# Optimization experiments

Hardware: AMD Instinct MI355X
Metric: run time of the kernel (lower is better)

The kernel has to match this reference:

```python
import jax, jax.numpy as jnp
import numpy as np

V, E, D, B, L1, L2, C, NL = 32000, 300, 256, 64, 128, 128, 3, 10
BN_EPS = 1e-3  # tf.layers.batch_normalization default epsilon
BN_SCALE = 1.0 / np.sqrt(1.0 + BN_EPS)  # inference BN with moving mean=0, var=1


def setup_inputs() -> dict:
    key = jax.random.key(0)
    ks = iter(jax.random.split(key, 32))
    g = lambda shape, s=0.05: jax.random.normal(next(ks), shape, jnp.float32) * s
    inp = dict(
        embed_table=g((V, E), 1.0),
        W1_first=g((E, D)),            # layer 1 linear-BN-ReLU-1 (input dim = embed dim)
        W1_rest=g((NL - 1, D, D)),     # layers 2..10 linear-BN-ReLU-1
        b1=jnp.zeros((NL, D)),
        bn1_g=jnp.ones((NL, D)), bn1_b=jnp.zeros((NL, D)),
        W2=g((NL, 2 * D, D)),          # linear-BN-ReLU-2 on [x, aligned] concat
        b2=jnp.zeros((NL, D)),
        bn2_g=jnp.ones((NL, D)), bn2_b=jnp.zeros((NL, D)),
        Wg=g((NL, D, D)), bg=jnp.zeros((NL, D)),  # sigmoid gate
        Wf1=g((4 * D, 4 * D), 0.01), bf1=jnp.zeros((4 * D,)),
        Wf2=g((4 * D, 4 * D), 0.01), bf2=jnp.zeros((4 * D,)),
        Wout=g((4 * D, C)), bout=jnp.zeros((C,)),
        x1_ids=jax.random.randint(next(ks), (B, L1), 0, V, dtype=jnp.int32),
        x2_ids=jax.random.randint(next(ks), (B, L2), 0, V, dtype=jnp.int32),
    )
    return inp


def _lbr(x, W, b, g, be):
    # linear -> BN (inference: moving mean 0, var 1) -> ReLU
    y = jnp.dot(x, W) + b
    y = g * (y * BN_SCALE) + be
    return jax.nn.relu(y)


def _block(x1, x2):
    # pairwise squared euclidean distance: |a-b|^2 = |a|^2 + |b|^2 - 2 a.b
    sq1 = jnp.sum(x1 * x1, -1)                                  # [B,L1]
    sq2 = jnp.sum(x2 * x2, -1)                                  # [B,L2]
    edist = sq1[:, :, None] + sq2[:, None, :] \
        - 2.0 * jnp.einsum('bid,bjd->bij', x1, x2)              # [B,L1,L2]
    att = 1.0 / (1.0 + edist)
    # alpha = softmax(att^T) @ x1 ; beta = softmax(att) @ x2
    alpha = jnp.einsum('bji,bid->bjd',
                       jax.nn.softmax(jnp.swapaxes(att, 1, 2), axis=-1), x1)  # [B,L2,D]
    beta = jnp.einsum('bij,bjd->bid', jax.nn.softmax(att, axis=-1), x2)       # [B,L1,D]
    return alpha, beta


def reference(embed_table, W1_first, W1_rest, b1, bn1_g, bn1_b,
              W2, b2, bn2_g, bn2_b, Wg, bg,
              Wf1, bf1, Wf2, bf2, Wout, bout, x1_ids, x2_ids):
    x1 = embed_table[x1_ids]  # [B,L1,E]
    x2 = embed_table[x2_ids]  # [B,L2,E]
    for i in range(NL):
        W1 = W1_first if i == 0 else W1_rest[i - 1]
        h1 = _lbr(x1, W1, b1[i], bn1_g[i], bn1_b[i])
        h2 = _lbr(x2, W1, b1[i], bn1_g[i], bn1_b[i])
        alpha, beta = _block(h1, h2)
        v1 = _lbr(jnp.concatenate([h1, beta], -1), W2[i], b2[i], bn2_g[i], bn2_b[i])
        v2 = _lbr(jnp.concatenate([h2, alpha], -1), W2[i], b2[i], bn2_g[i], bn2_b[i])
        g1 = jax.nn.sigmoid(jnp.dot(h1, Wg[i]) + bg[i])
        g2 = jax.nn.sigmoid(jnp.dot(h2, Wg[i]) + bg[i])
        x1 = v1 * g1 + h1 * (1.0 - g1)
        x2 = v2 * g2 + h2 * (1.0 - g2)
    v = jnp.concatenate([x1.max(1), x2.max(1), x1.sum(1), x2.sum(1)], -1)  # [B,4D]
    t = jax.nn.relu(jnp.dot(v, Wf1) + bf1)   # op.linear default activation (ReLU); dropout off
    t = jax.nn.relu(jnp.dot(t, Wf2) + bf2)
    return jnp.dot(t, Wout) + bout           # logits [B,C]
```

## Files before the change

kernel.cpp:

```cpp
#include <hip/hip_runtime.h>
#include <hip/hip_bf16.h>
#include <cstddef>

#define NB 64
#define LL 128
#define EE 300
#define DD 256
#define NLAYERS 10
#define MROWS (NB * LL)

static constexpr float BN_SC = 0.9995003746877562f;

typedef unsigned short u16;
typedef __attribute__((ext_vector_type(4))) unsigned short us4;
typedef __attribute__((ext_vector_type(8))) unsigned short us8;
typedef __attribute__((ext_vector_type(8))) short bfrag;
typedef __attribute__((ext_vector_type(4))) float f4;

#define MFMA_B16(a, b, c) __builtin_amdgcn_mfma_f32_16x16x32_bf16(a, b, c, 0, 0, 0)

__device__ __forceinline__ u16 f2bf(float x) {
  union { float f; unsigned u; } v; v.f = x;
  unsigned r = v.u + 0x7FFFu + ((v.u >> 16) & 1u);
  return (u16)(r >> 16);
}
__device__ __forceinline__ float bf2f(u16 s) {
  union { unsigned u; float f; } v; v.u = (unsigned)s << 16;
  return v.f;
}
__device__ __forceinline__ float4 ld4(const float* p) { return *(const float4*)p; }

__device__ __forceinline__ void async16(void* lds, const void* g) {
  __builtin_amdgcn_global_load_lds(
      (const __attribute__((address_space(1))) unsigned int*)g,
      (__attribute__((address_space(3))) unsigned int*)lds, 16, 0, 0);
}

__device__ __forceinline__ int swz64(int row, int colbyte) {
  return (row * 128 + colbyte) ^ ((row & 7) << 4);
}
__device__ __forceinline__ bfrag ldsT(const u16* T, int row, int colbyte) {
  return *(const bfrag*)((const char*)T + swz64(row, colbyte));
}

__device__ __forceinline__ void stage128x64(const u16* __restrict__ src, int ld,
                                            int r0, int k0, u16* lds, int t) {
  const int w = t >> 6;
#pragma unroll
  for (int j = 0; j < 4; ++j) {
    const int c = j * 256 + t;
    const int row = c >> 3, part = c & 7;
    const int sp = part ^ (row & 7);
    async16((char*)lds + j * 4096 + w * 1024,
            src + (size_t)(r0 + row) * ld + k0 + sp * 8);
  }
}
__device__ __forceinline__ void stage64x64(const u16* __restrict__ src, int ld,
                                           int r0, int k0, u16* lds, int t) {
  const int w = t >> 6;
#pragma unroll
  for (int j = 0; j < 2; ++j) {
    const int c = j * 256 + t;
    const int row = c >> 3, part = c & 7;
    const int sp = part ^ (row & 7);
    async16((char*)lds + j * 4096 + w * 1024,
            src + (size_t)(r0 + row) * ld + k0 + sp * 8);
  }
}

__device__ __forceinline__ void step_k64(const u16* As, const u16* Bs, int wm,
                                         int wn, int fr, int fq, f4 acc[4][2]) {
#pragma unroll
  for (int ks2 = 0; ks2 < 2; ++ks2) {
    bfrag a[4], b[2];
#pragma unroll
    for (int i = 0; i < 4; ++i)
      a[i] = ldsT(As, wm * 64 + i * 16 + fr, ks2 * 64 + fq * 16);
#pragma unroll
    for (int j = 0; j < 2; ++j)
      b[j] = ldsT(Bs, wn * 32 + j * 16 + fr, ks2 * 64 + fq * 16);
#pragma unroll
    for (int i = 0; i < 4; ++i)
#pragma unroll
      for (int j = 0; j < 2; ++j) acc[i][j] = MFMA_B16(a[i], b[j], acc[i][j]);
  }
}

__device__ __forceinline__ void step2_k64(const u16* As, const u16* B2s,
                                          const u16* Bgs, int wm, int wn,
                                          int fr, int fq, f4 accv[4][2],
                                          f4 accg[4][2]) {
#pragma unroll
  for (int ks2 = 0; ks2 < 2; ++ks2) {
    bfrag a[4], b2[2], bg[2];
#pragma unroll
    for (int i = 0; i < 4; ++i)
      a[i] = ldsT(As, wm * 64 + i * 16 + fr, ks2 * 64 + fq * 16);
#pragma unroll
    for (int j = 0; j < 2; ++j) {
      b2[j] = ldsT(B2s, wn * 32 + j * 16 + fr, ks2 * 64 + fq * 16);
      bg[j] = ldsT(Bgs, wn * 32 + j * 16 + fr, ks2 * 64 + fq * 16);
    }
#pragma unroll
    for (int i = 0; i < 4; ++i)
#pragma unroll
      for (int j = 0; j < 2; ++j) {
        accv[i][j] = MFMA_B16(a[i], b2[j], accv[i][j]);
        accg[i][j] = MFMA_B16(a[i], bg[j], accg[i][j]);
      }
  }
}

__device__ __forceinline__ bfrag gfrag(const u16* __restrict__ p, int ld, int row, int k) {
  return *(const bfrag*)(p + (size_t)row * ld + k);
}

__device__ __forceinline__ int eswz(int row, int colbyte) {
  return (row * 256 + colbyte) ^ ((row & 7) << 4);
}
__device__ __forceinline__ bfrag ldsE(const u16* E, int row, int colbyte) {
  return *(const bfrag*)((const char*)E + eswz(row, colbyte));
}

__device__ void txw_tile(const float* __restrict__ src, u16* __restrict__ dst,
                         int K, int N, int Kpad, int k0, int n0, int t,
                         float (*tileS)[65]) {
  __syncthreads();
  {
    const int kr = t >> 2, nc = (t & 3) * 16;
    const int k = k0 + kr;
#pragma unroll
    for (int j = 0; j < 16; j += 4) {
      float4 v = (k < K) ? ld4(src + (size_t)k * N + n0 + nc + j)
                         : make_float4(0.f, 0.f, 0.f, 0.f);
      tileS[kr][nc + j + 0] = v.x; tileS[kr][nc + j + 1] = v.y;
      tileS[kr][nc + j + 2] = v.z; tileS[kr][nc + j + 3] = v.w;
    }
  }
  __syncthreads();
  {
    const int nr = t >> 2, kc = (t & 3) * 16;
    us8 o0, o1;
#pragma unroll
    for (int j = 0; j < 8; ++j) {
      o0[j] = f2bf(tileS[kc + j][nr]);
      o1[j] = f2bf(tileS[kc + 8 + j][nr]);
    }
    u16* d = dst + (size_t)(n0 + nr) * Kpad + k0 + kc;
    *(us8*)d = o0;
    *(us8*)(d + 8) = o1;
  }
}

__global__ __launch_bounds__(256)
void k_prep(const float* __restrict__ W1f, const float* __restrict__ W1r,
            const float* __restrict__ W2, const float* __restrict__ Wg,
            const float* __restrict__ Wf1, const float* __restrict__ Wf2,
            u16* __restrict__ Wt1f, u16* __restrict__ Wt1r,
            u16* __restrict__ Wt2, u16* __restrict__ Wtg,
            u16* __restrict__ Wf1t, u16* __restrict__ Wf2t,
            const float* __restrict__ embed, const int* __restrict__ ids1,
            const int* __restrict__ ids2, u16* __restrict__ X1,
            u16* __restrict__ X2, u16* __restrict__ VPh, u16* __restrict__ VPl) {
  __shared__ float tileS[64][65];
  const int t = threadIdx.x;
  const int blk = blockIdx.x, nblk = gridDim.x;
  for (int it = blk; it < 20; it += nblk)
    txw_tile(W1f, Wt1f, 300, 256, 320, (it % 5) * 64, (it / 5) * 64, t, tileS);
  for (int it = blk; it < 144; it += nblk) {
    const int l = it / 16, r = it % 16;
    txw_tile(W1r + (size_t)l * 65536, Wt1r + (size_t)l * 65536, 256, 256, 256,
             (r % 4) * 64, (r / 4) * 64, t, tileS);
  }
  for (int it = blk; it < 320; it += nblk) {
    const int l = it / 32, r = it % 32;
    txw_tile(W2 + (size_t)l * 131072, Wt2 + (size_t)l * 131072, 512, 256, 512,
             (r % 8) * 64, (r / 8) * 64, t, tileS);
  }
  for (int it = blk; it < 160; it += nblk) {
    const int l = it / 16, r = it % 16;
    txw_tile(Wg + (size_t)l * 65536, Wtg + (size_t)l * 65536, 256, 256, 256,
             (r % 4) * 64, (r / 4) * 64, t, tileS);
  }
  for (int it = blk; it < 256; it += nblk)
    txw_tile(Wf1, Wf1t, 1024, 1024, 1024, (it % 16) * 64, (it / 16) * 64, t, tileS);
  for (int it = blk; it < 256; it += nblk)
    txw_tile(Wf2, Wf2t, 1024, 1024, 1024, (it % 16) * 64, (it / 16) * 64, t, tileS);
  for (int g = blk; g < 4096; g += nblk) {
    const int side = g & 1;
    const int* ids = side ? ids2 : ids1;
    u16* E = side ? X2 : X1;
    const int row = (g >> 1) * 4 + (t >> 6);
    const int lane = t & 63;
    const float* src = embed + (size_t)ids[row] * EE;
    u16* dst = E + (size_t)row * 320;
#pragma unroll
    for (int j = 0; j < 5; ++j) {
      const int c = lane + 64 * j;
      dst[c] = f2bf(c < EE ? src[c] : 0.f);
    }
  }
  for (int it = blk; it < 128; it += nblk) {
    const int arr = it & 1, row = 64 + (it >> 1);
    u16* dst = (arr ? VPl : VPh) + (size_t)row * 1024;
#pragma unroll
    for (int j = 0; j < 4; ++j) dst[t * 4 + j] = 0;
  }
}

__global__ __launch_bounds__(256, 2)
void mfma_lbr(const u16* __restrict__ A0, const u16* __restrict__ A1, int lda,
              int K, const u16* __restrict__ Wt, const float* __restrict__ bias,
              const float* __restrict__ gam, const float* __restrict__ bet,
              u16* __restrict__ O0, u16* __restrict__ O1,
              u16* __restrict__ HTa, u16* __restrict__ HTb,
              float* __restrict__ SQPa, float* __restrict__ SQPb) {
  const int side = blockIdx.z;
  const u16* A = side ? A1 : A0;
  u16* O = side ? O1 : O0;
  u16* HT = side ? HTb : HTa;
  float* SQP = side ? SQPb : SQPa;
  __shared__ u16 As[2][128 * 64], Bs[2][64 * 64];
  const int t = threadIdx.x;
  const int m0 = blockIdx.x * 128, n0 = blockIdx.y * 64;
  const int lane = t & 63, w = t >> 6, wm = w >> 1, wn = w & 1;
  const int fr = lane & 15, fq = lane >> 4;
  f4 acc[4][2] = {};
  const int nt = K / 64;
  stage128x64(A, lda, m0, 0, As[0], t);
  stage64x64(Wt, K, n0, 0, Bs[0], t);
  __syncthreads();
  for (int ks = 0; ks < nt; ++ks) {
    const int cur = ks & 1;
    if (ks + 1 < nt) {
      stage128x64(A, lda, m0, (ks + 1) * 64, As[cur ^ 1], t);
      stage64x64(Wt, K, n0, (ks + 1) * 64, Bs[cur ^ 1], t);
    }
    step_k64(As[cur], Bs[cur], wm, wn, fr, fq, acc);
    __syncthreads();
  }
  const int b = m0 >> 7;
  float rsq[4][4] = {};
#pragma unroll
  for (int nj = 0; nj < 2; ++nj) {
    const int n = n0 + wn * 32 + nj * 16 + fr;
    const float sc = gam[n] * BN_SC, bi = bias[n], be = bet[n];
#pragma unroll
    for (int mi = 0; mi < 4; ++mi) {
      const int m = m0 + wm * 64 + mi * 16 + fq * 4;
      us4 pk;
#pragma unroll
      for (int r = 0; r < 4; ++r) {
        const float x = sc * (acc[mi][nj][r] + bi) + be;
        const u16 hb = f2bf(fmaxf(x, 0.f));
        O[(size_t)(m + r) * DD + n] = hb;
        pk[r] = hb;
        const float h = bf2f(hb);
        rsq[mi][r] += h * h;
      }
      *(us4*)&HT[((size_t)b * DD + n) * LL + (m & 127)] = pk;
    }
  }
#pragma unroll
  for (int mi = 0; mi < 4; ++mi)
#pragma unroll
    for (int r = 0; r < 4; ++r) {
      float v = rsq[mi][r];
      v += __shfl_xor(v, 1, 64); v += __shfl_xor(v, 2, 64);
      v += __shfl_xor(v, 4, 64); v += __shfl_xor(v, 8, 64);
      rsq[mi][r] = v;
    }
  if (fr == 0) {
    const int p = blockIdx.y * 2 + wn;
#pragma unroll
    for (int mi = 0; mi < 4; ++mi)
#pragma unroll
      for (int r = 0; r < 4; ++r)
        SQP[(size_t)p * MROWS + m0 + wm * 64 + mi * 16 + fq * 4 + r] = rsq[mi][r];
  }
}

__global__ __launch_bounds__(256, 2)
void attf(const u16* __restrict__ H1, const u16* __restrict__ H2,
          const float* __restrict__ SQP1, const float* __restrict__ SQP2,
          const u16* __restrict__ HT1, const u16* __restrict__ HT2,
          u16* __restrict__ BETA, u16* __restrict__ ALPHA) {
  const int b = blockIdx.x, nh = blockIdx.y, side = blockIdx.z;
  __shared__ u16 Elds[128 * 128];
  __shared__ float sqs[2][128], rowp[2][128], colp[2][128];
  const int t = threadIdx.x, lane = t & 63, w = t >> 6;
  const int wm = w >> 1, wn = w & 1;
  const int fr = lane & 15, fq = lane >> 4;
  const int r0 = b * LL;
  if (t < 128) {
    float s = 0.f;
#pragma unroll
    for (int p = 0; p < 8; ++p) s += SQP1[(size_t)p * MROWS + r0 + t];
    sqs[0][t] = s;
  } else {
    const int u = t - 128;
    float s = 0.f;
#pragma unroll
    for (int p = 0; p < 8; ++p) s += SQP2[(size_t)p * MROWS + r0 + u];
    sqs[1][u] = s;
  }
  f4 acc[4][4] = {};
#pragma unroll
  for (int ks = 0; ks < 8; ++ks) {
    bfrag a[4], bv[4];
#pragma unroll
    for (int mi = 0; mi < 4; ++mi)
      a[mi] = gfrag(H1, DD, r0 + wm * 64 + mi * 16 + fr, ks * 32 + fq * 8);
#pragma unroll
    for (int nj = 0; nj < 4; ++nj)
      bv[nj] = gfrag(H2, DD, r0 + wn * 64 + nj * 16 + fr, ks * 32 + fq * 8);
#pragma unroll
    for (int mi = 0; mi < 4; ++mi)
#pragma unroll
      for (int nj = 0; nj < 4; ++nj) acc[mi][nj] = MFMA_B16(a[mi], bv[nj], acc[mi][nj]);
  }
  __syncthreads();
  float rp[4][4] = {}, cp[4] = {};
#pragma unroll
  for (int nj = 0; nj < 4; ++nj) {
    const int n = wn * 64 + nj * 16 + fr;
    const float s2 = sqs[1][n];
#pragma unroll
    for (int mi = 0; mi < 4; ++mi) {
      const int m = wm * 64 + mi * 16 + fq * 4;
#pragma unroll
      for (int r = 0; r < 4; ++r) {
        const float d = sqs[0][m + r] + s2 - 2.f * acc[mi][nj][r];
        const float e = __expf(1.f / (1.f + d));
        acc[mi][nj][r] = e;
        rp[mi][r] += e;
        cp[nj] += e;
      }
    }
  }
#pragma unroll
  for (int mi = 0; mi < 4; ++mi)
#pragma unroll
    for (int r = 0; r < 4; ++r) {
      float v = rp[mi][r];
      v += __shfl_xor(v, 1, 64); v += __shfl_xor(v, 2, 64);
      v += __shfl_xor(v, 4, 64); v += __shfl_xor(v, 8, 64);
      rp[mi][r] = v;
    }
#pragma unroll
  for (int nj = 0; nj < 4; ++nj) {
    float v = cp[nj];
    v += __shfl_xor(v, 16, 64); v += __shfl_xor(v, 32, 64);
    cp[nj] = v;
  }
  if (fr == 0)
#pragma unroll
    for (int mi = 0; mi < 4; ++mi)
#pragma unroll
      for (int r = 0; r < 4; ++r)
        rowp[wn][wm * 64 + mi * 16 + fq * 4 + r] = rp[mi][r];
  if (fq == 0)
#pragma unroll
    for (int nj = 0; nj < 4; ++nj)
      colp[wm][wn * 64 + nj * 16 + fr] = cp[nj];
  __syncthreads();
  if (side == 0) {
#pragma unroll
    for (int nj = 0; nj < 4; ++nj) {
      const int n = wn * 64 + nj * 16 + fr;
#pragma unroll
      for (int mi = 0; mi < 4; ++mi) {
        const int m = wm * 64 + mi * 16 + fq * 4;
#pragma unroll
        for (int r = 0; r < 4; ++r) {
          const float riv = 1.f / (rowp[0][m + r] + rowp[1][m + r]);
          *(u16*)((char*)Elds + eswz(m + r, n * 2)) = f2bf(acc[mi][nj][r] * riv);
        }
      }
    }
  } else {
#pragma unroll
    for (int nj = 0; nj < 4; ++nj) {
      const int n = wn * 64 + nj * 16 + fr;
      const float civ = 1.f / (colp[0][n] + colp[1][n]);
#pragma unroll
      for (int mi = 0; mi < 4; ++mi) {
        const int m = wm * 64 + mi * 16 + fq * 4;
        us4 pk;
#pragma unroll
        for (int r = 0; r < 4; ++r) pk[r] = f2bf(acc[mi][nj][r] * civ);
        *(us4*)((char*)Elds + eswz(n, m * 2)) = pk;
      }
    }
  }
  __syncthreads();
  const u16* HT = side ? HT1 : HT2;
  f4 pv[4][4] = {};
#pragma unroll
  for (int ks = 0; ks < 4; ++ks) {
    bfrag a[4], bv[4];
#pragma unroll
    for (int mi = 0; mi < 4; ++mi)
      a[mi] = ldsE(Elds, wm * 64 + mi * 16 + fr, ks * 64 + fq * 16);
#pragma unroll
    for (int nj = 0; nj < 4; ++nj)
      bv[nj] = gfrag(HT, LL, b * DD + nh * 128 + wn * 64 + nj * 16 + fr, ks * 32 + fq * 8);
#pragma unroll
    for (int mi = 0; mi < 4; ++mi)
#pragma unroll
      for (int nj = 0; nj < 4; ++nj) pv[mi][nj] = MFMA_B16(a[mi], bv[nj], pv[mi][nj]);
  }
  u16* O = side ? ALPHA : BETA;
#pragma unroll
  for (int nj = 0; nj < 4; ++nj) {
    const int n = nh * 128 + wn * 64 + nj * 16 + fr;
#pragma unroll
    for (int mi = 0; mi < 4; ++mi) {
      const int m = wm * 64 + mi * 16 + fq * 4;
#pragma unroll
      for (int r = 0; r < 4; ++r)
        O[(size_t)(r0 + m + r) * DD + n] = f2bf(pv[mi][nj][r]);
    }
  }
}

__global__ __launch_bounds__(256, 2)
void mfma_vg(const u16* __restrict__ Hbf1, const u16* __restrict__ Hbf2,
             const u16* __restrict__ BETA, const u16* __restrict__ ALPHA,
             const u16* __restrict__ Wt2, const u16* __restrict__ Wtg,
             const float* __restrict__ b2, const float* __restrict__ g2,
             const float* __restrict__ be2, const float* __restrict__ bgv,
             u16* __restrict__ X0, u16* __restrict__ X1p, int dopool,
             u16* __restrict__ VPh, u16* __restrict__ VPl) {
  const int side = blockIdx.z;
  const u16* H = side ? Hbf2 : Hbf1;
  const u16* CC = side ? ALPHA : BETA;
  u16* X = side ? X1p : X0;
  const int m0 = blockIdx.x * 128, n0 = blockIdx.y * 64;
  __shared__ u16 As[2][128 * 64], B2s[2][64 * 64], Bgs[2][64 * 64];
  __shared__ float pmx[2][64], psm[2][64];
  const int t = threadIdx.x;
  const int lane = t & 63, w = t >> 6, wm = w >> 1, wn = w & 1;
  const int fr = lane & 15, fq = lane >> 4;
  f4 accv[4][2] = {}, accg[4][2] = {};
  stage128x64(H, DD, m0, 0, As[0], t);
  stage64x64(Wt2, 2 * DD, n0, 0, B2s[0], t);
  stage64x64(Wtg, DD, n0, 0, Bgs[0], t);
  __syncthreads();
  for (int ks = 0; ks < 8; ++ks) {
    const int cur = ks & 1;
    if (ks + 1 < 8) {
      const u16* Asrc = (ks + 1 < 4) ? H : CC;
      stage128x64(Asrc, DD, m0, ((ks + 1) & 3) * 64, As[cur ^ 1], t);
      stage64x64(Wt2, 2 * DD, n0, (ks + 1) * 64, B2s[cur ^ 1], t);
      if (ks + 1 < 4) stage64x64(Wtg, DD, n0, (ks + 1) * 64, Bgs[cur ^ 1], t);
    }
    if (ks < 4)
      step2_k64(As[cur], B2s[cur], Bgs[cur], wm, wn, fr, fq, accv, accg);
    else
      step_k64(As[cur], B2s[cur], wm, wn, fr, fq, accv);
    __syncthreads();
  }
  float pmax[2] = {-1e30f, -1e30f}, psum[2] = {0.f, 0.f};
#pragma unroll
  for (int nj = 0; nj < 2; ++nj) {
    const int n = n0 + wn * 32 + nj * 16 + fr;
    const float sc = g2[n] * BN_SC, bi = b2[n], be = be2[n], bgn = bgv[n];
#pragma unroll
    for (int mi = 0; mi < 4; ++mi) {
      const int m = m0 + wm * 64 + mi * 16 + fq * 4;
#pragma unroll
      for (int r = 0; r < 4; ++r) {
        const float v = fmaxf(sc * (accv[mi][nj][r] + bi) + be, 0.f);
        const float g = 1.f / (1.f + __expf(-(accg[mi][nj][r] + bgn)));
        const float h = bf2f(H[(size_t)(m + r) * DD + n]);
        const u16 xb = f2bf(v * g + h * (1.f - g));
        X[(size_t)(m + r) * DD + n] = xb;
        if (dopool) {
          const float xv = bf2f(xb);
          pmax[nj] = fmaxf(pmax[nj], xv);
          psum[nj] += xv;
        }
      }
    }
  }
  if (dopool) {
#pragma unroll
    for (int nj = 0; nj < 2; ++nj) {
      float mx = pmax[nj], sm = psum[nj];
      mx = fmaxf(mx, __shfl_xor(mx, 16, 64)); sm += __shfl_xor(sm, 16, 64);
      mx = fmaxf(mx, __shfl_xor(mx, 32, 64)); sm += __shfl_xor(sm, 32, 64);
      if (fq == 0) {
        pmx[wm][wn * 32 + nj * 16 + fr] = mx;
        psm[wm][wn * 32 + nj * 16 + fr] = sm;
      }
    }
    __syncthreads();
    if (t < 64) {
      const float mx = fmaxf(pmx[0][t], pmx[1][t]);
      const float sm = psm[0][t] + psm[1][t];
      const int b = m0 >> 7;
      const int col = n0 + t;
      const u16 mh = f2bf(mx);
      VPh[(size_t)b * 1024 + side * 256 + col] = mh;
      VPl[(size_t)b * 1024 + side * 256 + col] = f2bf(mx - bf2f(mh));
      const u16 sh = f2bf(sm);
      VPh[(size_t)b * 1024 + (2 + side) * 256 + col] = sh;
      VPl[(size_t)b * 1024 + (2 + side) * 256 + col] = f2bf(sm - bf2f(sh));
    }
  }
}

__global__ __launch_bounds__(256, 2)
void mlp_sk(const u16* __restrict__ Ah, const u16* __restrict__ Al,
            const u16* __restrict__ Wt, float* __restrict__ PART) {
  const int n0 = blockIdx.x * 128;
  const int k0 = blockIdx.y * 128;
  const int t = threadIdx.x, lane = t & 63, w = t >> 6;
  const int wm = w >> 1, wn = w & 1;
  const int fr = lane & 15, fq = lane >> 4;
  f4 acc[4][4] = {};
#pragma unroll
  for (int ks = 0; ks < 4; ++ks) {
    bfrag ah[4], al[4], bv[4];
#pragma unroll
    for (int mi = 0; mi < 4; ++mi) {
      ah[mi] = gfrag(Ah, 1024, wm * 64 + mi * 16 + fr, k0 + ks * 32 + fq * 8);
      al[mi] = gfrag(Al, 1024, wm * 64 + mi * 16 + fr, k0 + ks * 32 + fq * 8);
    }
#pragma unroll
    for (int nj = 0; nj < 4; ++nj)
      bv[nj] = gfrag(Wt, 1024, n0 + wn * 64 + nj * 16 + fr, k0 + ks * 32 + fq * 8);
#pragma unroll
    for (int mi = 0; mi < 4; ++mi)
#pragma unroll
      for (int nj = 0; nj < 4; ++nj) {
        acc[mi][nj] = MFMA_B16(ah[mi], bv[nj], acc[mi][nj]);
        acc[mi][nj] = MFMA_B16(al[mi], bv[nj], acc[mi][nj]);
      }
  }
#pragma unroll
  for (int nj = 0; nj < 4; ++nj) {
    const int n = n0 + wn * 64 + nj * 16 + fr;
#pragma unroll
    for (int mi = 0; mi < 4; ++mi) {
      const int m = wm * 64 + mi * 16 + fq * 4;
#pragma unroll
      for (int r = 0; r < 4; ++r)
        PART[((size_t)blockIdx.y * 128 + m + r) * 1024 + n] = acc[mi][nj][r];
    }
  }
}

__global__ __launch_bounds__(512)
void mlp_comb(const float* __restrict__ P, const float* __restrict__ bias,
              u16* __restrict__ Oh, u16* __restrict__ Ol) {
#pragma unroll
  for (int e = 0; e < 8; ++e) {
    const int idx = blockIdx.x * 4096 + e * 512 + threadIdx.x;
    const int col = idx & 1023;
    float s = bias[col];
#pragma unroll
    for (int p = 0; p < 8; ++p) s += P[(size_t)p * 131072 + idx];
    s = fmaxf(s, 0.f);
    const u16 h = f2bf(s);
    Oh[idx] = h;
    Ol[idx] = f2bf(s - bf2f(h));
  }
}

__global__ __launch_bounds__(512)
void mlp_comb_out(const float* __restrict__ P, const float* __restrict__ bias,
                  const float* __restrict__ Wout, const float* __restrict__ bout,
                  float* __restrict__ out) {
  __shared__ float red[4][8][3];
  const int t = threadIdx.x;
  float a[4][3] = {};
#pragma unroll
  for (int e = 0; e < 8; ++e) {
    const int idx = blockIdx.x * 4096 + e * 512 + t;
    const int col = idx & 1023;
    float s = bias[col];
#pragma unroll
    for (int p = 0; p < 8; ++p) s += P[(size_t)p * 131072 + idx];
    s = fmaxf(s, 0.f);
    const int lr = e >> 1;
    a[lr][0] = fmaf(s, Wout[col * 3 + 0], a[lr][0]);
    a[lr][1] = fmaf(s, Wout[col * 3 + 1], a[lr][1]);
    a[lr][2] = fmaf(s, Wout[col * 3 + 2], a[lr][2]);
  }
  const int lane = t & 63, w = t >> 6;
#pragma unroll
  for (int lr = 0; lr < 4; ++lr)
#pragma unroll
    for (int c = 0; c < 3; ++c) {
      float v = a[lr][c];
#pragma unroll
      for (int off = 32; off > 0; off >>= 1) v += __shfl_down(v, off, 64);
      if (lane == 0) red[lr][w][c] = v;
    }
  __syncthreads();
  if (t < 12) {
    const int lr = t / 3, c = t % 3;
    float s = bout[c];
#pragma unroll
    for (int w8 = 0; w8 < 8; ++w8) s += red[lr][w8][c];
    out[(blockIdx.x * 4 + lr) * 3 + c] = s;
  }
}

extern "C" void kernel_launch(void* const* d_in, const int* in_sizes, int n_in,
                              void* d_out, int out_size, void* d_ws, size_t ws_size,
                              hipStream_t stream) {
  (void)in_sizes; (void)n_in; (void)out_size; (void)ws_size;
  const float* embed = (const float*)d_in[0];
  const float* W1f   = (const float*)d_in[1];
  const float* W1r   = (const float*)d_in[2];
  const float* b1    = (const float*)d_in[3];
  const float* bn1g  = (const float*)d_in[4];
  const float* bn1b  = (const float*)d_in[5];
  const float* W2    = (const float*)d_in[6];
  const float* b2    = (const float*)d_in[7];
  const float* bn2g  = (const float*)d_in[8];
  const float* bn2b  = (const float*)d_in[9];
  const float* Wg    = (const float*)d_in[10];
  const float* bg    = (const float*)d_in[11];
  const float* Wf1   = (const float*)d_in[12];
  const float* bf1   = (const float*)d_in[13];
  const float* Wf2   = (const float*)d_in[14];
  const float* bf2   = (const float*)d_in[15];
  const float* Wout  = (const float*)d_in[16];
  const float* bout  = (const float*)d_in[17];
  const int* ids1    = (const int*)d_in[18];
  const int* ids2    = (const int*)d_in[19];

  char* wsp = (char*)d_ws;
  auto alloc = [&](size_t bytes) {
    char* p = wsp;
    wsp += (bytes + 255) & ~(size_t)255;
    return p;
  };
  u16* Hbf1  = (u16*)alloc((size_t)MROWS * DD * 2);
  u16* Hbf2  = (u16*)alloc((size_t)MROWS * DD * 2);
  u16* HT1   = (u16*)alloc((size_t)MROWS * DD * 2);
  u16* HT2   = (u16*)alloc((size_t)MROWS * DD * 2);
  u16* Xbf1  = (u16*)alloc((size_t)MROWS * 320 * 2);
  u16* Xbf2  = (u16*)alloc((size_t)MROWS * 320 * 2);
  u16* BETAb = (u16*)alloc((size_t)MROWS * DD * 2);
  u16* ALPHAb= (u16*)alloc((size_t)MROWS * DD * 2);
  float* SQP1= (float*)alloc((size_t)8 * MROWS * 4);
  float* SQP2= (float*)alloc((size_t)8 * MROWS * 4);
  u16* Wt1f  = (u16*)alloc((size_t)DD * 320 * 2);
  u16* Wt1r  = (u16*)alloc((size_t)9 * DD * DD * 2);
  u16* Wt2   = (u16*)alloc((size_t)10 * DD * 2 * DD * 2);
  u16* Wtg   = (u16*)alloc((size_t)10 * DD * DD * 2);
  u16* Wf1t  = (u16*)alloc((size_t)1024 * 1024 * 2);
  u16* Wf2t  = (u16*)alloc((size_t)1024 * 1024 * 2);
  u16* VPh   = (u16*)alloc((size_t)128 * 1024 * 2);
  u16* VPl   = (u16*)alloc((size_t)128 * 1024 * 2);
  u16* T1h   = (u16*)alloc((size_t)128 * 1024 * 2);
  u16* T1l   = (u16*)alloc((size_t)128 * 1024 * 2);
  float* PART1 = (float*)alloc((size_t)8 * 128 * 1024 * 4);
  float* PART2 = (float*)alloc((size_t)8 * 128 * 1024 * 4);

  k_prep<<<512, 256, 0, stream>>>(W1f, W1r, W2, Wg, Wf1, Wf2,
                                  Wt1f, Wt1r, Wt2, Wtg, Wf1t, Wf2t,
                                  embed, ids1, ids2, Xbf1, Xbf2, VPh, VPl);

  for (int i = 0; i < NLAYERS; ++i) {
    const u16* Wt1 = (i == 0) ? Wt1f : (Wt1r + (size_t)(i - 1) * DD * DD);
    const int K1 = (i == 0) ? 320 : DD;
    mfma_lbr<<<dim3(MROWS / 128, 4, 2), 256, 0, stream>>>(
        Xbf1, Xbf2, K1, K1, Wt1, b1 + i * DD, bn1g + i * DD, bn1b + i * DD,
        Hbf1, Hbf2, HT1, HT2, SQP1, SQP2);
    attf<<<dim3(NB, 2, 2), 256, 0, stream>>>(Hbf1, Hbf2, SQP1, SQP2, HT1, HT2,
                                             BETAb, ALPHAb);
    mfma_vg<<<dim3(MROWS / 128, 4, 2), 256, 0, stream>>>(
        Hbf1, Hbf2, BETAb, ALPHAb, Wt2 + (size_t)i * DD * 2 * DD,
        Wtg + (size_t)i * DD * DD, b2 + i * DD, bn2g + i * DD, bn2b + i * DD,
        bg + i * DD, Xbf1, Xbf2, (i == NLAYERS - 1) ? 1 : 0, VPh, VPl);
  }
  mlp_sk<<<dim3(8, 8), 256, 0, stream>>>(VPh, VPl, Wf1t, PART1);
  mlp_comb<<<32, 512, 0, stream>>>(PART1, bf1, T1h, T1l);
  mlp_sk<<<dim3(8, 8), 256, 0, stream>>>(T1h, T1l, Wf2t, PART2);
  mlp_comb_out<<<16, 512, 0, stream>>>(PART2, bf2, Wout, bout, (float*)d_out);
}
```

Baseline: 491.1 us.

## Triple-buffer mfma_lbr staging and drop split-K from the final MLP

In mfma_lbr, staging moves from double to triple buffering. Two K tiles are prefetched ahead, with explicit vmcnt waits and a single barrier per step, so global loads overlap more with MFMA work. The final MLP also drops split-K: each of 8 blocks now runs the full K=1024 reduction and applies bias and ReLU in-kernel, and a small per-row kernel computes the output projection. This removes the partial-sum buffers and the combine kernels, but leaves only 8 blocks doing long serial K loops, so the MLP may lose parallelism.

```diff
diff --git a/kernel.cpp b/kernel.cpp
--- a/kernel.cpp
+++ b/kernel.cpp
@@ -220,7 +220,7 @@
   u16* O = side ? O1 : O0;
   u16* HT = side ? HTb : HTa;
   float* SQP = side ? SQPb : SQPa;
-  __shared__ u16 As[2][128 * 64], Bs[2][64 * 64];
+  __shared__ u16 As[3][128 * 64], Bs[3][64 * 64];
   const int t = threadIdx.x;
   const int m0 = blockIdx.x * 128, n0 = blockIdx.y * 64;
   const int lane = t & 63, w = t >> 6, wm = w >> 1, wn = w & 1;
@@ -229,15 +229,18 @@
   const int nt = K / 64;
   stage128x64(A, lda, m0, 0, As[0], t);
   stage64x64(Wt, K, n0, 0, Bs[0], t);
-  __syncthreads();
+  stage128x64(A, lda, m0, 64, As[1], t);
+  stage64x64(Wt, K, n0, 64, Bs[1], t);
   for (int ks = 0; ks < nt; ++ks) {
-    const int cur = ks & 1;
-    if (ks + 1 < nt) {
-      stage128x64(A, lda, m0, (ks + 1) * 64, As[cur ^ 1], t);
-      stage64x64(Wt, K, n0, (ks + 1) * 64, Bs[cur ^ 1], t);
-    }
-    step_k64(As[cur], Bs[cur], wm, wn, fr, fq, acc);
-    __syncthreads();
+    if (ks < nt - 1) asm volatile("s_waitcnt vmcnt(6)" ::: "memory");
+    else             asm volatile("s_waitcnt vmcnt(0)" ::: "memory");
+    __builtin_amdgcn_sched_barrier(0);
+    __builtin_amdgcn_s_barrier();
+    if (ks + 2 < nt) {
+      stage128x64(A, lda, m0, (ks + 2) * 64, As[(ks + 2) % 3], t);
+      stage64x64(Wt, K, n0, (ks + 2) * 64, Bs[(ks + 2) % 3], t);
+    }
+    step_k64(As[ks % 3], Bs[ks % 3], wm, wn, fr, fq, acc);
   }
   const int b = m0 >> 7;
   float rsq[4][4] = {};
@@ -512,25 +515,26 @@
 }
 
 __global__ __launch_bounds__(256, 2)
-void mlp_sk(const u16* __restrict__ Ah, const u16* __restrict__ Al,
-            const u16* __restrict__ Wt, float* __restrict__ PART) {
+void mlp_full(const u16* __restrict__ Ah, const u16* __restrict__ Al,
+              const u16* __restrict__ Wt, const float* __restrict__ bias,
+              u16* __restrict__ Oh, u16* __restrict__ Ol,
+              float* __restrict__ Of) {
   const int n0 = blockIdx.x * 128;
-  const int k0 = blockIdx.y * 128;
   const int t = threadIdx.x, lane = t & 63, w = t >> 6;
   const int wm = w >> 1, wn = w & 1;
   const int fr = lane & 15, fq = lane >> 4;
   f4 acc[4][4] = {};
-#pragma unroll
-  for (int ks = 0; ks < 4; ++ks) {
+#pragma unroll 4
+  for (int ks = 0; ks < 32; ++ks) {
     bfrag ah[4], al[4], bv[4];
 #pragma unroll
     for (int mi = 0; mi < 4; ++mi) {
-      ah[mi] = gfrag(Ah, 1024, wm * 64 + mi * 16 + fr, k0 + ks * 32 + fq * 8);
-      al[mi] = gfrag(Al, 1024, wm * 64 + mi * 16 + fr, k0 + ks * 32 + fq * 8);
+      ah[mi] = gfrag(Ah, 1024, wm * 64 + mi * 16 + fr, ks * 32 + fq * 8);
+      al[mi] = gfrag(Al, 1024, wm * 64 + mi * 16 + fr, ks * 32 + fq * 8);
     }
 #pragma unroll
     for (int nj = 0; nj < 4; ++nj)
-      bv[nj] = gfrag(Wt, 1024, n0 + wn * 64 + nj * 16 + fr, k0 + ks * 32 + fq * 8);
+      bv[nj] = gfrag(Wt, 1024, n0 + wn * 64 + nj * 16 + fr, ks * 32 + fq * 8);
 #pragma unroll
     for (int mi = 0; mi < 4; ++mi)
 #pragma unroll
@@ -542,71 +546,49 @@
 #pragma unroll
   for (int nj = 0; nj < 4; ++nj) {
     const int n = n0 + wn * 64 + nj * 16 + fr;
+    const float bi = bias[n];
 #pragma unroll
     for (int mi = 0; mi < 4; ++mi) {
       const int m = wm * 64 + mi * 16 + fq * 4;
 #pragma unroll
-      for (int r = 0; r < 4; ++r)
-        PART[((size_t)blockIdx.y * 128 + m + r) * 1024 + n] = acc[mi][nj][r];
-    }
-  }
-}
-
-__global__ __launch_bounds__(512)
-void mlp_comb(const float* __restrict__ P, const float* __restrict__ bias,
-              u16* __restrict__ Oh, u16* __restrict__ Ol) {
-#pragma unroll
-  for (int e = 0; e < 8; ++e) {
-    const int idx = blockIdx.x * 4096 + e * 512 + threadIdx.x;
-    const int col = idx & 1023;
-    float s = bias[col];
-#pragma unroll
-    for (int p = 0; p < 8; ++p) s += P[(size_t)p * 131072 + idx];
-    s = fmaxf(s, 0.f);
-    const u16 h = f2bf(s);
-    Oh[idx] = h;
-    Ol[idx] = f2bf(s - bf2f(h));
-  }
-}
-
-__global__ __launch_bounds__(512)
-void mlp_comb_out(const float* __restrict__ P, const float* __restrict__ bias,
-                  const float* __restrict__ Wout, const float* __restrict__ bout,
-                  float* __restrict__ out) {
-  __shared__ float red[4][8][3];
+      for (int r = 0; r < 4; ++r) {
+        const float v = fmaxf(acc[mi][nj][r] + bi, 0.f);
+        if (Oh) {
+          const u16 h = f2bf(v);
+          Oh[(size_t)(m + r) * 1024 + n] = h;
+          Ol[(size_t)(m + r) * 1024 + n] = f2bf(v - bf2f(h));
+        } else {
+          Of[(size_t)(m + r) * 1024 + n] = v;
+        }
+      }
+    }
+  }
+}
+
+__global__ __launch_bounds__(256)
+void out_kernel(const float* __restrict__ T2, const float* __restrict__ Wout,
+                const float* __restrict__ bout, float* __restrict__ out) {
+  const int b = blockIdx.x;
   const int t = threadIdx.x;
-  float a[4][3] = {};
-#pragma unroll
-  for (int e = 0; e < 8; ++e) {
-    const int idx = blockIdx.x * 4096 + e * 512 + t;
-    const int col = idx & 1023;
-    float s = bias[col];
-#pragma unroll
-    for (int p = 0; p < 8; ++p) s += P[(size_t)p * 131072 + idx];
-    s = fmaxf(s, 0.f);
-    const int lr = e >> 1;
-    a[lr][0] = fmaf(s, Wout[col * 3 + 0], a[lr][0]);
-    a[lr][1] = fmaf(s, Wout[col * 3 + 1], a[lr][1]);
-    a[lr][2] = fmaf(s, Wout[col * 3 + 2], a[lr][2]);
-  }
-  const int lane = t & 63, w = t >> 6;
-#pragma unroll
-  for (int lr = 0; lr < 4; ++lr)
-#pragma unroll
-    for (int c = 0; c < 3; ++c) {
-      float v = a[lr][c];
-#pragma unroll
-      for (int off = 32; off > 0; off >>= 1) v += __shfl_down(v, off, 64);
-      if (lane == 0) red[lr][w][c] = v;
-    }
+  float a0 = 0.f, a1 = 0.f, a2 = 0.f;
+  for (int k = t; k < 1024; k += 256) {
+    const float x = T2[(size_t)b * 1024 + k];
+    a0 = fmaf(x, Wout[k * 3 + 0], a0);
+    a1 = fmaf(x, Wout[k * 3 + 1], a1);
+    a2 = fmaf(x, Wout[k * 3 + 2], a2);
+  }
+  __shared__ float red[3][256];
+  red[0][t] = a0; red[1][t] = a1; red[2][t] = a2;
   __syncthreads();
-  if (t < 12) {
-    const int lr = t / 3, c = t % 3;
-    float s = bout[c];
-#pragma unroll
-    for (int w8 = 0; w8 < 8; ++w8) s += red[lr][w8][c];
-    out[(blockIdx.x * 4 + lr) * 3 + c] = s;
-  }
+  for (int off = 128; off > 0; off >>= 1) {
+    if (t < off) {
+      red[0][t] += red[0][t + off];
+      red[1][t] += red[1][t + off];
+      red[2][t] += red[2][t + off];
+    }
+    __syncthreads();
+  }
+  if (t < 3) out[b * 3 + t] = red[t][0] + bout[t];
 }
 
 extern "C" void kernel_launch(void* const* d_in, const int* in_sizes, int n_in,
@@ -660,8 +642,7 @@
   u16* VPl   = (u16*)alloc((size_t)128 * 1024 * 2);
   u16* T1h   = (u16*)alloc((size_t)128 * 1024 * 2);
   u16* T1l   = (u16*)alloc((size_t)128 * 1024 * 2);
-  float* PART1 = (float*)alloc((size_t)8 * 128 * 1024 * 4);
-  float* PART2 = (float*)alloc((size_t)8 * 128 * 1024 * 4);
+  float* T2f = (float*)alloc((size_t)128 * 1024 * 4);
 
   k_prep<<<512, 256, 0, stream>>>(W1f, W1r, W2, Wg, Wf1, Wf2,
                                   Wt1f, Wt1r, Wt2, Wtg, Wf1t, Wf2t,
@@ -680,8 +661,7 @@
         Wtg + (size_t)i * DD * DD, b2 + i * DD, bn2g + i * DD, bn2b + i * DD,
         bg + i * DD, Xbf1, Xbf2, (i == NLAYERS - 1) ? 1 : 0, VPh, VPl);
   }
-  mlp_sk<<<dim3(8, 8), 256, 0, stream>>>(VPh, VPl, Wf1t, PART1);
-  mlp_comb<<<32, 512, 0, stream>>>(PART1, bf1, T1h, T1l);
-  mlp_sk<<<dim3(8, 8), 256, 0, stream>>>(T1h, T1l, Wf2t, PART2);
-  mlp_comb_out<<<16, 512, 0, stream>>>(PART2, bf2, Wout, bout, (float*)d_out);
-}
+  mlp_full<<<8, 256, 0, stream>>>(VPh, VPl, Wf1t, bf1, T1h, T1l, nullptr);
+  mlp_full<<<8, 256, 0, stream>>>(T1h, T1l, Wf2t, bf2, nullptr, nullptr, T2f);
+  out_kernel<<<NB, 256, 0, stream>>>(T2f, Wout, bout, (float*)d_out);
+}
```

After: 596.1 us. +21.4%, slower.
